# Optimization experiments

Hardware: AMD Instinct MI355X
Metric: run time of the kernel (lower is better)

The kernel has to match this reference:

```python
import jax, jax.numpy as jnp
import numpy as np

B, T, IN, H, L = 32, 512, 8, 1024, 3


def _gru_layer(x, W_ih, W_hh, b_ih, b_hh):
    # x: [B,T,D_in]; W_ih: [3H,D_in]; W_hh: [3H,H]; gate order r,z,n (PyTorch)
    Bx = x.shape[0]
    Hh = W_hh.shape[1]
    xg = jnp.einsum('btd,gd->btg', x, W_ih) + b_ih  # [B,T,3H] input-side gates, precomputed

    def step(h, xg_t):
        hg = h @ W_hh.T + b_hh
        xr, xz, xn = jnp.split(xg_t, 3, axis=-1)
        hr, hz, hn = jnp.split(hg, 3, axis=-1)
        r = jax.nn.sigmoid(xr + hr)
        z = jax.nn.sigmoid(xz + hz)
        n = jnp.tanh(xn + r * hn)
        h_new = (1.0 - z) * n + z * h
        return h_new, h_new

    h0 = jnp.zeros((Bx, Hh), x.dtype)
    _, ys = jax.lax.scan(step, h0, jnp.swapaxes(xg, 0, 1))  # [T,B,H]
    return jnp.swapaxes(ys, 0, 1)  # [B,T,H]


def setup_inputs() -> dict:
    key = jax.random.key(0)
    ks = jax.random.split(key, 32)
    k = 1.0 / np.sqrt(H)

    def u(kk, shape):
        return jax.random.uniform(kk, shape, jnp.float32, -k, k)

    inp = {'x': jax.random.normal(ks[0], (B, T, IN), jnp.float32)}
    i = 1
    for l in range(L):
        d_in = IN if l == 0 else H
        inp[f'W_ih{l}'] = u(ks[i], (3 * H, d_in)); i += 1
        inp[f'W_hh{l}'] = u(ks[i], (3 * H, H)); i += 1
        inp[f'b_ih{l}'] = u(ks[i], (3 * H,)); i += 1
        inp[f'b_hh{l}'] = u(ks[i], (3 * H,)); i += 1
    inp['fc1_w'] = u(ks[i], (512, H)); i += 1
    inp['fc1_b'] = u(ks[i], (512,)); i += 1
    inp['fc2_w'] = u(ks[i], (256, 512)); i += 1
    inp['fc2_b'] = u(ks[i], (256,)); i += 1
    inp['fc3_w'] = u(ks[i], (1, 256)); i += 1
    inp['fc3_b'] = u(ks[i], (1,)); i += 1
    return inp


def reference(x, W_ih0, W_hh0, b_ih0, b_hh0, W_ih1, W_hh1, b_ih1, b_hh1,
              W_ih2, W_hh2, b_ih2, b_hh2, fc1_w, fc1_b, fc2_w, fc2_b, fc3_w, fc3_b):
    h = x
    h = _gru_layer(h, W_ih0, W_hh0, b_ih0, b_hh0)
    h = _gru_layer(h, W_ih1, W_hh1, b_ih1, b_hh1)
    h = _gru_layer(h, W_ih2, W_hh2, b_ih2, b_hh2)
    h = jnp.mean(h, axis=1)  # temporal mean-pool -> [B,H]
    h = jax.nn.relu(h @ fc1_w.T + fc1_b)
    h = jax.nn.relu(h @ fc2_w.T + fc2_b)
    return h @ fc3_w.T + fc3_b  # [B,1]
```

## Files before the change

kernel.cpp:

```cpp
#include <hip/hip_runtime.h>
#include <cmath>

#define TT 512
#define BB 32
#define HH 1024
#define G3 3072

__device__ __forceinline__ void mv_phase(
    float (*wAll)[HH],
    float* stgL,
    float (*part)[12][32],
    const float* __restrict__ src,
    int wrow, int tid)
{
    const int wv = tid >> 6, l = tid & 63;
    const int ks = l >> 3, bg = l & 7;
    float acc[12][4];
#pragma unroll
    for (int r = 0; r < 12; r++) {
        acc[r][0] = 0.f; acc[r][1] = 0.f; acc[r][2] = 0.f; acc[r][3] = 0.f;
    }

    float4 ld[4];
#pragma unroll
    for (int i = 0; i < 4; i++)
        ld[i] = *(const float4*)&src[(size_t)(i * 8 + wv) * HH + l * 4];

#pragma unroll
    for (int c = 0; c < 4; c++) {
        __syncthreads();
#pragma unroll
        for (int i = 0; i < 4; i++) {
            int b = i * 8 + wv;
            *(float4*)&stgL[b * 256 + ((l ^ ((b >> 2) & 7)) << 2)] = ld[i];
        }
        __syncthreads();
        if (c < 3) {
#pragma unroll
            for (int i = 0; i < 4; i++)
                ld[i] = *(const float4*)&src[(size_t)(i * 8 + wv) * HH + (c + 1) * 256 + l * 4];
        }
        const int kw = c * 256 + wv * 32 + ks * 4;
        const int kb = wv * 8 + ks;
        float4 h4[4];
#pragma unroll
        for (int e = 0; e < 4; e++) {
            int b = bg * 4 + e;
            h4[e] = *(const float4*)&stgL[b * 256 + ((kb ^ ((b >> 2) & 7)) << 2)];
        }
#pragma unroll
        for (int r = 0; r < 12; r++) {
            float4 w4 = *(const float4*)&wAll[wrow + r][kw];
#pragma unroll
            for (int e = 0; e < 4; e++) {
                acc[r][e] = fmaf(w4.x, h4[e].x, acc[r][e]);
                acc[r][e] = fmaf(w4.y, h4[e].y, acc[r][e]);
                acc[r][e] = fmaf(w4.z, h4[e].z, acc[r][e]);
                acc[r][e] = fmaf(w4.w, h4[e].w, acc[r][e]);
            }
        }
    }
#pragma unroll
    for (int r = 0; r < 12; r++)
#pragma unroll
        for (int e = 0; e < 4; e++) {
            float v = acc[r][e];
            v += __shfl_xor(v, 16, 64);
            v += __shfl_xor(v, 32, 64);
            acc[r][e] = v;
        }
    if (l < 16) {
        int s = l >> 3, bgw = l & 7;
#pragma unroll
        for (int r = 0; r < 12; r++) {
            float4 o = make_float4(acc[r][0], acc[r][1], acc[r][2], acc[r][3]);
            *(float4*)&part[wv * 2 + s][r][bgw * 4] = o;
        }
    }
}

template<int IN_DIM>
__global__ __launch_bounds__(512, 2) void k_scan(
    const float* __restrict__ xsrc,
    const float* __restrict__ Wih,
    const float* __restrict__ Whh,
    const float* __restrict__ bih,
    const float* __restrict__ bhh,
    float* __restrict__ y,
    int* __restrict__ barx,
    float* __restrict__ pool)
{
    __shared__ float wAll[24][HH];
    __shared__ float stgL[32 * 256];
    __shared__ float part[16][12][32];
    __shared__ float bi[12], bh[12];
    __shared__ double pool_l[128];

    const int tid = threadIdx.x;
    const int j0 = blockIdx.x * 4;

    for (int i = tid; i < 12 * 256; i += 512) {
        int r = i >> 8, c4 = (i & 255) * 4;
        int g = r >> 2, jj = r & 3;
        *(float4*)&wAll[r][c4] =
            *(const float4*)&Whh[(size_t)(g * HH + j0 + jj) * HH + c4];
    }
    if (IN_DIM == HH) {
        for (int i = tid; i < 12 * 256; i += 512) {
            int r = i >> 8, c4 = (i & 255) * 4;
            int g = r >> 2, jj = r & 3;
            *(float4*)&wAll[12 + r][c4] =
                *(const float4*)&Wih[(size_t)(g * HH + j0 + jj) * HH + c4];
        }
    } else {
        if (tid < 96) {
            int r = tid >> 3, d = tid & 7;
            int g = r >> 2, jj = r & 3;
            wAll[12 + r][d] = Wih[(size_t)(g * HH + j0 + jj) * IN_DIM + d];
        }
    }
    if (tid < 12) {
        int g = tid >> 2, jj = tid & 3;
        bi[tid] = bih[g * HH + j0 + jj];
        bh[tid] = bhh[g * HH + j0 + jj];
    }
    if (tid < 128) pool_l[tid] = 0.0;
    __syncthreads();

    float hp_reg = 0.f;
    for (int t = 0; t < TT; t++) {
        double ig0 = 0.0, ig1 = 0.0, ig2 = 0.0;
        if (IN_DIM == HH) {
            mv_phase(wAll, stgL, part, xsrc + (size_t)t * BB * HH, 12, tid);
            __syncthreads();
            if (tid < 128) {
                int b = tid >> 2, jj = tid & 3;
                ig0 = bi[jj]; ig1 = bi[4 + jj]; ig2 = bi[8 + jj];
#pragma unroll
                for (int p = 0; p < 16; p++) {
                    ig0 += part[p][jj][b];
                    ig1 += part[p][4 + jj][b];
                    ig2 += part[p][8 + jj][b];
                }
            }
        }
        if (t > 0) {
            if (tid < 8) {
                const int target = 32 * t;
                while (__hip_atomic_load(&barx[tid * 16], __ATOMIC_RELAXED,
                                         __HIP_MEMORY_SCOPE_AGENT) < target)
                    __builtin_amdgcn_s_sleep(1);
            }
            __syncthreads();
            mv_phase(wAll, stgL, part, y + (size_t)(t - 1) * BB * HH, 0, tid);
            __syncthreads();
        }
        if (tid < 128) {
            int b = tid >> 2, jj = tid & 3, jg = j0 + jj;
            double hg0 = bh[jj], hg1 = bh[4 + jj], hg2 = bh[8 + jj];
            if (t > 0) {
#pragma unroll
                for (int p = 0; p < 16; p++) {
                    hg0 += part[p][jj][b];
                    hg1 += part[p][4 + jj][b];
                    hg2 += part[p][8 + jj][b];
                }
            }
            if (IN_DIM != HH) {
                const float* xp = xsrc + ((size_t)b * TT + t) * IN_DIM;
                float xv[8];
                *(float4*)&xv[0] = *(const float4*)&xp[0];
                *(float4*)&xv[4] = *(const float4*)&xp[4];
                float s0 = 0.f, s1 = 0.f, s2 = 0.f;
#pragma unroll
                for (int d = 0; d < 8; d++) {
                    s0 = fmaf(wAll[12 + jj][d], xv[d], s0);
                    s1 = fmaf(wAll[16 + jj][d], xv[d], s1);
                    s2 = fmaf(wAll[20 + jj][d], xv[d], s2);
                }
                ig0 = (double)bi[jj] + s0;
                ig1 = (double)bi[4 + jj] + s1;
                ig2 = (double)bi[8 + jj] + s2;
            }
            float rr = 1.f / (1.f + expf(-(float)(ig0 + hg0)));
            float zz = 1.f / (1.f + expf(-(float)(ig1 + hg1)));
            float nn = tanhf((float)(ig2 + (double)rr * hg2));
            float hnew = (1.f - zz) * nn + zz * hp_reg;
            hp_reg = hnew;
            __hip_atomic_store(&y[(size_t)t * BB * HH + b * HH + jg], hnew,
                               __ATOMIC_RELAXED, __HIP_MEMORY_SCOPE_AGENT);
            if (pool != nullptr) pool_l[tid] += (double)hnew;
        }
        if (t < TT - 1) {
            __syncthreads();
            if (tid == 0)
                __hip_atomic_fetch_add(&barx[(blockIdx.x & 7) * 16], 1,
                                       __ATOMIC_RELAXED, __HIP_MEMORY_SCOPE_AGENT);
        }
    }
    __syncthreads();
    if (pool != nullptr && tid < 128) {
        int b = tid >> 2, jj = tid & 3;
        pool[b * HH + j0 + jj] = (float)(pool_l[tid] * (1.0 / 512.0));
    }
}

__global__ __launch_bounds__(512, 1) void k_scan_x(
    const float* __restrict__ xg,
    const float* __restrict__ Whh,
    const float* __restrict__ bhh,
    float* __restrict__ y,
    int* __restrict__ flagx,
    double* __restrict__ pool,
    int t0, int t1)
{
    __shared__ float wAll[12][HH];
    __shared__ float part[16][12][32];
    __shared__ float bh[12];
    __shared__ double pool_l[128];

    const int tid = threadIdx.x;
    const int j0 = blockIdx.x * 4;
    const int wv = tid >> 6, l = tid & 63;
    const int ks = l >> 3, bg = l & 7;

    for (int i = tid; i < 12 * 256; i += 512) {
        int r = i >> 8, c4 = (i & 255) * 4;
        int g = r >> 2, jj = r & 3;
        *(float4*)&wAll[r][c4] =
            *(const float4*)&Whh[(size_t)(g * HH + j0 + jj) * HH + c4];
    }
    if (tid < 12) bh[tid] = bhh[(tid >> 2) * HH + j0 + (tid & 3)];
    if (tid < 128) pool_l[tid] = 0.0;

    const int gb = tid >> 2, gjj = tid & 3;
    float hp_reg = 0.f;
    if (t0 > 0 && tid < 128)
        hp_reg = y[(size_t)(t0 - 1) * BB * HH + gb * HH + j0 + gjj];
    __syncthreads();

    for (int t = t0; t < t1; t++) {
        float xr = 0.f, xz = 0.f, xn = 0.f;
        if (tid < 128) {
            const float* xrow = xg + ((size_t)(t - t0) * BB + gb) * G3;
            xr = xrow[j0 + gjj];
            xz = xrow[HH + j0 + gjj];
            xn = xrow[2 * HH + j0 + gjj];
        }
        if (t > t0) {
            if (tid < 64) {
                const int target = t - t0;
                const int* fp = flagx + tid * 4;
                for (;;) {
                    int f0 = __hip_atomic_load(fp + 0, __ATOMIC_RELAXED,
                                               __HIP_MEMORY_SCOPE_AGENT);
                    int f1 = __hip_atomic_load(fp + 1, __ATOMIC_RELAXED,
                                               __HIP_MEMORY_SCOPE_AGENT);
                    int f2 = __hip_atomic_load(fp + 2, __ATOMIC_RELAXED,
                                               __HIP_MEMORY_SCOPE_AGENT);
                    int f3 = __hip_atomic_load(fp + 3, __ATOMIC_RELAXED,
                                               __HIP_MEMORY_SCOPE_AGENT);
                    int m01 = f0 < f1 ? f0 : f1;
                    int m23 = f2 < f3 ? f2 : f3;
                    int m = m01 < m23 ? m01 : m23;
                    if (__all(m >= target)) break;
                    __builtin_amdgcn_s_sleep(1);
                }
            }
            __syncthreads();
        }
        if (t > 0) {
            const float* hsrc = y + (size_t)(t - 1) * BB * HH;
            float4 hr[4][4];
#pragma unroll
            for (int c = 0; c < 4; c++)
#pragma unroll
                for (int e = 0; e < 4; e++)
                    hr[c][e] = *(const float4*)
                        &hsrc[(size_t)(bg * 4 + e) * HH + c * 256 + wv * 32 + ks * 4];

            float acc[12][4];
#pragma unroll
            for (int r = 0; r < 12; r++) {
                acc[r][0] = 0.f; acc[r][1] = 0.f; acc[r][2] = 0.f; acc[r][3] = 0.f;
            }
#pragma unroll
            for (int c = 0; c < 4; c++) {
                const int kw = c * 256 + wv * 32 + ks * 4;
#pragma unroll
                for (int r = 0; r < 12; r++) {
                    float4 w4 = *(const float4*)&wAll[r][kw];
#pragma unroll
                    for (int e = 0; e < 4; e++) {
                        acc[r][e] = fmaf(w4.x, hr[c][e].x, acc[r][e]);
                        acc[r][e] = fmaf(w4.y, hr[c][e].y, acc[r][e]);
                        acc[r][e] = fmaf(w4.z, hr[c][e].z, acc[r][e]);
                        acc[r][e] = fmaf(w4.w, hr[c][e].w, acc[r][e]);
                    }
                }
            }
#pragma unroll
            for (int r = 0; r < 12; r++)
#pragma unroll
                for (int e = 0; e < 4; e++) {
                    float v = acc[r][e];
                    v += __shfl_xor(v, 16, 64);
                    v += __shfl_xor(v, 32, 64);
                    acc[r][e] = v;
                }
            if (l < 16) {
                int s = l >> 3, bgw = l & 7;
#pragma unroll
                for (int r = 0; r < 12; r++) {
                    float4 o = make_float4(acc[r][0], acc[r][1], acc[r][2], acc[r][3]);
                    *(float4*)&part[wv * 2 + s][r][bgw * 4] = o;
                }
            }
            __syncthreads();
        }
        if (tid < 128) {
            double hg0 = bh[gjj], hg1 = bh[4 + gjj], hg2 = bh[8 + gjj];
            if (t > 0) {
#pragma unroll
                for (int p = 0; p < 16; p++) {
                    hg0 += part[p][gjj][gb];
                    hg1 += part[p][4 + gjj][gb];
                    hg2 += part[p][8 + gjj][gb];
                }
            }
            float rr = 1.f / (1.f + expf(-(xr + (float)hg0)));
            float zz = 1.f / (1.f + expf(-(xz + (float)hg1)));
            float nn = tanhf(xn + rr * (float)hg2);
            float hnew = (1.f - zz) * nn + zz * hp_reg;
            hp_reg = hnew;
            __hip_atomic_store(&y[(size_t)t * BB * HH + gb * HH + j0 + gjj], hnew,
                               __ATOMIC_RELAXED, __HIP_MEMORY_SCOPE_AGENT);
            if (pool != nullptr) pool_l[tid] += (double)hnew;
        }
        if (t < t1 - 1) {
            __syncthreads();
            if (tid == 0)
                __hip_atomic_store(&flagx[blockIdx.x], t - t0 + 1,
                                   __ATOMIC_RELAXED, __HIP_MEMORY_SCOPE_AGENT);
        }
    }
    __syncthreads();
    if (pool != nullptr && tid < 128)
        pool[gb * HH + j0 + gjj] += pool_l[tid];
}

__global__ __launch_bounds__(512) void k_poolfin(const double* __restrict__ pd,
                                                 float* __restrict__ pf)
{
    int i = blockIdx.x * 512 + threadIdx.x;
    if (i < BB * HH) pf[i] = (float)(pd[i] * (1.0 / 512.0));
}

__global__ __launch_bounds__(256, 2) void k_gemm_xg(const float* __restrict__ A,
                                                    const float* __restrict__ Bw,
                                                    const float* __restrict__ bias,
                                                    float* __restrict__ C)
{
    __shared__ float As[16][132];
    __shared__ float Bs[16][132];
    const int tid = threadIdx.x;
    const int tx = tid & 15, ty = tid >> 4;
    const int bm = blockIdx.x * 128, bn = blockIdx.y * 128;
    float acc[8][8];
#pragma unroll
    for (int i = 0; i < 8; i++)
#pragma unroll
        for (int j = 0; j < 8; j++) acc[i][j] = 0.f;

    const int srow = tid >> 1, sch = (tid & 1) * 8;
    for (int k0 = 0; k0 < HH; k0 += 16) {
        {
            const float* ap = &A[(size_t)(bm + srow) * HH + k0 + sch];
            float4 v0 = *(const float4*)ap;
            float4 v1 = *(const float4*)(ap + 4);
            As[sch + 0][srow] = v0.x; As[sch + 1][srow] = v0.y;
            As[sch + 2][srow] = v0.z; As[sch + 3][srow] = v0.w;
            As[sch + 4][srow] = v1.x; As[sch + 5][srow] = v1.y;
            As[sch + 6][srow] = v1.z; As[sch + 7][srow] = v1.w;
            const float* bp = &Bw[(size_t)(bn + srow) * HH + k0 + sch];
            float4 u0 = *(const float4*)bp;
            float4 u1 = *(const float4*)(bp + 4);
            Bs[sch + 0][srow] = u0.x; Bs[sch + 1][srow] = u0.y;
            Bs[sch + 2][srow] = u0.z; Bs[sch + 3][srow] = u0.w;
            Bs[sch + 4][srow] = u1.x; Bs[sch + 5][srow] = u1.y;
            Bs[sch + 6][srow] = u1.z; Bs[sch + 7][srow] = u1.w;
        }
        __syncthreads();
#pragma unroll
        for (int k = 0; k < 16; k++) {
            float a[8], b[8];
            *(float4*)&a[0] = *(const float4*)&As[k][ty * 8];
            *(float4*)&a[4] = *(const float4*)&As[k][ty * 8 + 4];
            *(float4*)&b[0] = *(const float4*)&Bs[k][tx * 8];
            *(float4*)&b[4] = *(const float4*)&Bs[k][tx * 8 + 4];
#pragma unroll
            for (int i = 0; i < 8; i++)
#pragma unroll
                for (int j = 0; j < 8; j++)
                    acc[i][j] = fmaf(a[i], b[j], acc[i][j]);
        }
        __syncthreads();
    }
#pragma unroll
    for (int i = 0; i < 8; i++) {
        float o[8];
#pragma unroll
        for (int j = 0; j < 8; j++) o[j] = acc[i][j] + bias[bn + tx * 8 + j];
        float* cp = &C[(size_t)(bm + ty * 8 + i) * G3 + bn + tx * 8];
        *(float4*)cp = *(float4*)&o[0];
        *(float4*)(cp + 4) = *(float4*)&o[4];
    }
}

__global__ __launch_bounds__(256) void k_gemm_xg0(const float* __restrict__ x,
                                                  const float* __restrict__ W,
                                                  const float* __restrict__ bias,
                                                  float* __restrict__ C,
                                                  int t0)
{
    __shared__ float As[128][8];
    __shared__ float Bs[128][8];
    const int tid = threadIdx.x;
    const int bm = blockIdx.x * 128, bn = blockIdx.y * 128;
    {
        int r = tid >> 1, hf = (tid & 1) * 4;
        int m = bm + r;
        int b = m & 31, tt = t0 + (m >> 5);
        *(float4*)&As[r][hf] = *(const float4*)&x[((size_t)b * TT + tt) * 8 + hf];
        *(float4*)&Bs[r][hf] = *(const float4*)&W[(size_t)(bn + r) * 8 + hf];
    }
    __syncthreads();
    const int tx = tid & 15, ty = tid >> 4;
    float acc[8][8];
#pragma unroll
    for (int i = 0; i < 8; i++)
#pragma unroll
        for (int j = 0; j < 8; j++) acc[i][j] = 0.f;
#pragma unroll
    for (int k = 0; k < 8; k++) {
        float a[8], b[8];
#pragma unroll
        for (int i = 0; i < 8; i++) a[i] = As[ty * 8 + i][k];
#pragma unroll
        for (int j = 0; j < 8; j++) b[j] = Bs[tx * 8 + j][k];
#pragma unroll
        for (int i = 0; i < 8; i++)
#pragma unroll
            for (int j = 0; j < 8; j++)
                acc[i][j] = fmaf(a[i], b[j], acc[i][j]);
    }
#pragma unroll
    for (int i = 0; i < 8; i++) {
        float o[8];
#pragma unroll
        for (int j = 0; j < 8; j++) o[j] = acc[i][j] + bias[bn + tx * 8 + j];
        float* cp = &C[(size_t)(bm + ty * 8 + i) * G3 + bn + tx * 8];
        *(float4*)cp = *(float4*)&o[0];
        *(float4*)(cp + 4) = *(float4*)&o[4];
    }
}

__global__ __launch_bounds__(256) void k_fc(const float* __restrict__ in,
                                            const float* __restrict__ w,
                                            const float* __restrict__ bias,
                                            float* __restrict__ out,
                                            int ind, int outd, int dorelu)
{
    int b = blockIdx.y;
    int o = blockIdx.x * 256 + threadIdx.x;
    if (o >= outd) return;
    const float* ip = in + (size_t)b * ind;
    const float* wp = w + (size_t)o * ind;
    double s = (double)bias[o];
    for (int k = 0; k < ind; k += 4) {
        float4 wv = *(const float4*)&wp[k];
        float4 iv = *(const float4*)&ip[k];
        s += (double)iv.x * wv.x + (double)iv.y * wv.y
           + (double)iv.z * wv.z + (double)iv.w * wv.w;
    }
    float v = (float)s;
    if (dorelu) v = fmaxf(v, 0.f);
    out[(size_t)b * outd + o] = v;
}

extern "C" void kernel_launch(void* const* d_in, const int* in_sizes, int n_in,
                              void* d_out, int out_size, void* d_ws, size_t ws_size,
                              hipStream_t stream)
{
    (void)in_sizes; (void)n_in; (void)out_size;
    const float* x    = (const float*)d_in[0];
    const float* Wih[3] = {(const float*)d_in[1], (const float*)d_in[5], (const float*)d_in[9]};
    const float* Whh[3] = {(const float*)d_in[2], (const float*)d_in[6], (const float*)d_in[10]};
    const float* bih[3] = {(const float*)d_in[3], (const float*)d_in[7], (const float*)d_in[11]};
    const float* bhh[3] = {(const float*)d_in[4], (const float*)d_in[8], (const float*)d_in[12]};
    const float* fc1w = (const float*)d_in[13];
    const float* fc1b = (const float*)d_in[14];
    const float* fc2w = (const float*)d_in[15];
    const float* fc2b = (const float*)d_in[16];
    const float* fc3w = (const float*)d_in[17];
    const float* fc3b = (const float*)d_in[18];

    int*    bars     = (int*)d_ws;
    int*    flags    = bars + 96 * 128;
    double* pooled_d = (double*)(flags + 96 * 256);
    float*  pooled_f = (float*)(pooled_d + BB * HH);
    float*  fc1o     = pooled_f + BB * HH;
    float*  fc2o     = fc1o + BB * 512;
    float*  y0       = fc2o + BB * 256;
    float*  y1       = y0 + (size_t)TT * BB * HH;
    float*  xg       = y1 + (size_t)TT * BB * HH;

    const size_t base = (size_t)((char*)xg - (char*)d_ws);
    if (ws_size < base) return;

    int CH = 0;
    for (int c = 512; c >= 16; c >>= 1) {
        if (base + (size_t)c * BB * G3 * 4 <= ws_size) { CH = c; break; }
    }

    hipMemsetAsync(bars, 0, (96 * 128 + 96 * 256) * sizeof(int), stream);
    hipMemsetAsync(pooled_d, 0, BB * HH * sizeof(double), stream);

    int binst = 0;
    if (CH > 0) {
        for (int t0 = 0; t0 < TT; t0 += CH) {
            k_gemm_xg0<<<dim3(CH * BB / 128, G3 / 128), 256, 0, stream>>>(
                x, Wih[0], bih[0], xg, t0);
            k_scan_x<<<256, 512, 0, stream>>>(
                xg, Whh[0], bhh[0], y0, flags + (binst++) * 256, nullptr, t0, t0 + CH);
        }
        float* ybuf[2] = {y0, y1};
        for (int l = 1; l <= 2; l++) {
            const float* src = ybuf[(l - 1) & 1];
            float* dst = ybuf[l & 1];
            double* pl = (l == 2) ? pooled_d : nullptr;
            for (int t0 = 0; t0 < TT; t0 += CH) {
                k_gemm_xg<<<dim3(CH * BB / 128, G3 / 128), 256, 0, stream>>>(
                    src + (size_t)t0 * BB * HH, Wih[l], bih[l], xg);
                k_scan_x<<<256, 512, 0, stream>>>(
                    xg, Whh[l], bhh[l], dst, flags + (binst++) * 256, pl, t0, t0 + CH);
            }
        }
        k_poolfin<<<(BB * HH + 511) / 512, 512, 0, stream>>>(pooled_d, pooled_f);
        k_fc<<<dim3(2, 32), 256, 0, stream>>>(pooled_f, fc1w, fc1b, fc1o, HH, 512, 1);
    } else {
        float* pooled_fb = pooled_f;
        k_scan<8><<<256, 512, 0, stream>>>(x, Wih[0], Whh[0], bih[0], bhh[0], y0,
                                           bars + (binst++) * 128, nullptr);
        k_scan<HH><<<256, 512, 0, stream>>>(y0, Wih[1], Whh[1], bih[1], bhh[1], y1,
                                            bars + (binst++) * 128, nullptr);
        k_scan<HH><<<256, 512, 0, stream>>>(y1, Wih[2], Whh[2], bih[2], bhh[2], y0,
                                            bars + (binst++) * 128, pooled_fb);
        k_fc<<<dim3(2, 32), 256, 0, stream>>>(pooled_fb, fc1w, fc1b, fc1o, HH, 512, 1);
    }

    k_fc<<<dim3(1, 32), 256, 0, stream>>>(fc1o, fc2w, fc2b, fc2o, 512, 256, 1);
    k_fc<<<dim3(1, 32), 256, 0, stream>>>(fc2o, fc3w, fc3b, (float*)d_out, 256, 1, 0);
}
```

Baseline: 16.33 ms.

## Confine gate update to one wavefront and drop the per-step block barrier

The gate-combine and state-update work moves from 128 threads (two wavefronts) to 64 threads, each handling two hidden units. Because the writers now sit in a single wavefront, the per-step __syncthreads before publishing the progress flag is replaced by an s_waitcnt vmcnt(0) inside that wavefront. Pool accumulation also moves from shared memory into registers. The aim is to cut block-wide barrier latency on the serial recurrence's critical path. In exchange, each lane does twice the transcendental math, and the ordering of other wavefronts now relies on barriers elsewhere in the loop.

```diff
diff --git a/kernel.cpp b/kernel.cpp
--- a/kernel.cpp
+++ b/kernel.cpp
@@ -217,7 +217,6 @@
     __shared__ float wAll[12][HH];
     __shared__ float part[16][12][32];
     __shared__ float bh[12];
-    __shared__ double pool_l[128];
 
     const int tid = threadIdx.x;
     const int j0 = blockIdx.x * 4;
@@ -231,21 +230,24 @@
             *(const float4*)&Whh[(size_t)(g * HH + j0 + jj) * HH + c4];
     }
     if (tid < 12) bh[tid] = bhh[(tid >> 2) * HH + j0 + (tid & 3)];
-    if (tid < 128) pool_l[tid] = 0.0;
-
-    const int gb = tid >> 2, gjj = tid & 3;
-    float hp_reg = 0.f;
-    if (t0 > 0 && tid < 128)
-        hp_reg = y[(size_t)(t0 - 1) * BB * HH + gb * HH + j0 + gjj];
+
+    const int b2 = tid >> 1, jb = (tid & 1) * 2;
+    float hp0 = 0.f, hp1 = 0.f;
+    double pacc0 = 0.0, pacc1 = 0.0;
+    if (t0 > 0 && tid < 64) {
+        hp0 = y[(size_t)(t0 - 1) * BB * HH + b2 * HH + j0 + jb];
+        hp1 = y[(size_t)(t0 - 1) * BB * HH + b2 * HH + j0 + jb + 1];
+    }
     __syncthreads();
 
     for (int t = t0; t < t1; t++) {
-        float xr = 0.f, xz = 0.f, xn = 0.f;
-        if (tid < 128) {
-            const float* xrow = xg + ((size_t)(t - t0) * BB + gb) * G3;
-            xr = xrow[j0 + gjj];
-            xz = xrow[HH + j0 + gjj];
-            xn = xrow[2 * HH + j0 + gjj];
+        float xr0 = 0.f, xz0 = 0.f, xn0 = 0.f;
+        float xr1 = 0.f, xz1 = 0.f, xn1 = 0.f;
+        if (tid < 64) {
+            const float* xrow = xg + ((size_t)(t - t0) * BB + b2) * G3;
+            xr0 = xrow[j0 + jb];          xr1 = xrow[j0 + jb + 1];
+            xz0 = xrow[HH + j0 + jb];     xz1 = xrow[HH + j0 + jb + 1];
+            xn0 = xrow[2 * HH + j0 + jb]; xn1 = xrow[2 * HH + j0 + jb + 1];
         }
         if (t > t0) {
             if (tid < 64) {
@@ -318,35 +320,45 @@
             }
             __syncthreads();
         }
-        if (tid < 128) {
-            double hg0 = bh[gjj], hg1 = bh[4 + gjj], hg2 = bh[8 + gjj];
+        if (tid < 64) {
+            double hgA0 = bh[jb], hgA1 = bh[4 + jb], hgA2 = bh[8 + jb];
+            double hgB0 = bh[jb + 1], hgB1 = bh[4 + jb + 1], hgB2 = bh[8 + jb + 1];
             if (t > 0) {
 #pragma unroll
                 for (int p = 0; p < 16; p++) {
-                    hg0 += part[p][gjj][gb];
-                    hg1 += part[p][4 + gjj][gb];
-                    hg2 += part[p][8 + gjj][gb];
-                }
-            }
-            float rr = 1.f / (1.f + expf(-(xr + (float)hg0)));
-            float zz = 1.f / (1.f + expf(-(xz + (float)hg1)));
-            float nn = tanhf(xn + rr * (float)hg2);
-            float hnew = (1.f - zz) * nn + zz * hp_reg;
-            hp_reg = hnew;
-            __hip_atomic_store(&y[(size_t)t * BB * HH + gb * HH + j0 + gjj], hnew,
-                               __ATOMIC_RELAXED, __HIP_MEMORY_SCOPE_AGENT);
-            if (pool != nullptr) pool_l[tid] += (double)hnew;
-        }
-        if (t < t1 - 1) {
-            __syncthreads();
-            if (tid == 0)
-                __hip_atomic_store(&flagx[blockIdx.x], t - t0 + 1,
-                                   __ATOMIC_RELAXED, __HIP_MEMORY_SCOPE_AGENT);
-        }
-    }
-    __syncthreads();
-    if (pool != nullptr && tid < 128)
-        pool[gb * HH + j0 + gjj] += pool_l[tid];
+                    hgA0 += part[p][jb][b2];
+                    hgA1 += part[p][4 + jb][b2];
+                    hgA2 += part[p][8 + jb][b2];
+                    hgB0 += part[p][jb + 1][b2];
+                    hgB1 += part[p][4 + jb + 1][b2];
+                    hgB2 += part[p][8 + jb + 1][b2];
+                }
+            }
+            float rA = 1.f / (1.f + expf(-(xr0 + (float)hgA0)));
+            float zA = 1.f / (1.f + expf(-(xz0 + (float)hgA1)));
+            float nA = tanhf(xn0 + rA * (float)hgA2);
+            float h0 = (1.f - zA) * nA + zA * hp0;
+            float rB = 1.f / (1.f + expf(-(xr1 + (float)hgB0)));
+            float zB = 1.f / (1.f + expf(-(xz1 + (float)hgB1)));
+            float nB = tanhf(xn1 + rB * (float)hgB2);
+            float h1 = (1.f - zB) * nB + zB * hp1;
+            hp0 = h0; hp1 = h1;
+            float* yrow = y + (size_t)t * BB * HH + b2 * HH + j0 + jb;
+            __hip_atomic_store(yrow, h0, __ATOMIC_RELAXED, __HIP_MEMORY_SCOPE_AGENT);
+            __hip_atomic_store(yrow + 1, h1, __ATOMIC_RELAXED, __HIP_MEMORY_SCOPE_AGENT);
+            if (pool != nullptr) { pacc0 += (double)h0; pacc1 += (double)h1; }
+            if (t < t1 - 1) {
+                asm volatile("s_waitcnt vmcnt(0)" ::: "memory");
+                if (tid == 0)
+                    __hip_atomic_store(&flagx[blockIdx.x], t - t0 + 1,
+                                       __ATOMIC_RELAXED, __HIP_MEMORY_SCOPE_AGENT);
+            }
+        }
+    }
+    if (pool != nullptr && tid < 64) {
+        pool[b2 * HH + j0 + jb]     += pacc0;
+        pool[b2 * HH + j0 + jb + 1] += pacc1;
+    }
 }
 
 __global__ __launch_bounds__(512) void k_poolfin(const double* __restrict__ pd,
```

New measurement: 18.53 ms. 13.4% more time.
